# Performance work log

Measured on AMD Instinct MI355X. Metric: run time of the kernel, lower is better.

The kernel has to match this reference:

```python
import jax, jax.numpy as jnp
import numpy as np

P = 524288          # total sampled points
N_RAYS = 4096       # rays
N_FREQ = 5
N_FREQ_VIEW = 3
ACT_SHIFT = float(np.log(1.0 / (1.0 - 0.1) - 1.0))  # alpha_init = 0.1
INTERVAL = 0.5      # stepsize * voxel_size_ratio


def sin_emb(x, n_freq):
    # x: (M,3) -> (M, 3 + 6*n_freq): [x, sin(2^i x), cos(2^i x)]
    freqs = 2.0 ** jnp.arange(n_freq, dtype=x.dtype)
    parts = [x]
    for f in freqs:
        parts.append(jnp.sin(f * x))
        parts.append(jnp.cos(f * x))
    return jnp.concatenate(parts, axis=1)


def _pipeline(sampling_coor, sampling_view, raw_density, ray_id,
              wb0, bb0, wb1, bb1, wb2, bb2,
              wa0, ba0, wa1, ba1, wa2, ba2,
              w_lat, b_lat, w_view, b_view, w_c0, b_c0, w_c1, b_c1):
    relu = jax.nn.relu
    emb = sin_emb(sampling_coor, N_FREQ)                    # (P, 33)
    view_emb = sin_emb(sampling_view, N_FREQ_VIEW)[ray_id]  # (P, 21)
    # Decoder_woslot (K == 1)
    h = relu(emb @ wb0 + bb0)
    h = relu(h @ wb1 + bb1)
    h = relu(h @ wb2 + bb2)
    h = jnp.concatenate([emb, h], axis=1)                   # skip: (P, 97)
    h = relu(h @ wa0 + ba0)
    h = relu(h @ wa1 + ba1)
    h = relu(h @ wa2 + ba2)
    latent = h @ w_lat + b_lat                              # (P, 64)
    hv = relu(jnp.concatenate([latent, view_emb], axis=1) @ w_view + b_view)
    rgb_raw = relu(hv @ w_c0 + b_c0) @ w_c1 + b_c1          # (P, 3)
    rgb = (jnp.tanh(rgb_raw) + 1.0) * 0.5
    sigma = jax.nn.softplus(raw_density[0] + ACT_SHIFT)     # (P,)
    # Raw2Alpha: alpha = 1 - exp(-sigma*interval); hence log(1-alpha) = -sigma*interval
    alpha = 1.0 - jnp.exp(-sigma * INTERVAL)
    log_t = -sigma * INTERVAL
    # Alphas2Weights: per-ray exclusive cumprod of (1-alpha); ray_id is sorted
    cl = jnp.cumsum(log_t)
    excl = cl - log_t                                        # exclusive global cumsum
    base = jax.ops.segment_max(excl, ray_id, num_segments=N_RAYS)  # value at each ray start
    T = jnp.exp(excl - base[ray_id])                         # transmittance
    weights = T * alpha                                      # (P,)
    alphainv_last = jnp.exp(jax.ops.segment_sum(log_t, ray_id, num_segments=N_RAYS))
    # composite with white background
    rgb_marched = (jax.ops.segment_sum(weights[:, None] * rgb, ray_id, num_segments=N_RAYS)
                   + alphainv_last[:, None])
    return rgb_marched                                       # (N_RAYS, 3)


def setup_inputs() -> dict:
    key = jax.random.key(0)
    ks = iter(jax.random.split(key, 40))

    def w(fi, fo):
        return jax.random.normal(next(ks), (fi, fo), jnp.float32) / np.sqrt(fi).astype(np.float32)

    inp = {
        'sampling_coor': jax.random.normal(next(ks), (P, 3), jnp.float32),
        'sampling_view': jax.random.normal(next(ks), (N_RAYS, 3), jnp.float32),
        'raw_density': jax.random.normal(next(ks), (1, P), jnp.float32),
        'ray_id': jnp.sort(jax.random.randint(next(ks), (P,), 0, N_RAYS, jnp.int32)),
        'wb0': w(33, 64), 'bb0': jnp.zeros((64,), jnp.float32),
        'wb1': w(64, 64), 'bb1': jnp.zeros((64,), jnp.float32),
        'wb2': w(64, 64), 'bb2': jnp.zeros((64,), jnp.float32),
        'wa0': w(97, 64), 'ba0': jnp.zeros((64,), jnp.float32),
        'wa1': w(64, 64), 'ba1': jnp.zeros((64,), jnp.float32),
        'wa2': w(64, 64), 'ba2': jnp.zeros((64,), jnp.float32),
        'w_lat': w(64, 64), 'b_lat': jnp.zeros((64,), jnp.float32),
        'w_view': w(85, 32), 'b_view': jnp.zeros((32,), jnp.float32),
        'w_c0': w(32, 16), 'b_c0': jnp.zeros((16,), jnp.float32),
        'w_c1': w(16, 3), 'b_c1': jnp.zeros((3,), jnp.float32),
    }
    return inp


def reference(sampling_coor, sampling_view, raw_density, ray_id,
              wb0, bb0, wb1, bb1, wb2, bb2,
              wa0, ba0, wa1, ba1, wa2, ba2,
              w_lat, b_lat, w_view, b_view, w_c0, b_c0, w_c1, b_c1):
    return _pipeline(sampling_coor, sampling_view, raw_density, ray_id,
                     wb0, bb0, wb1, bb1, wb2, bb2,
                     wa0, ba0, wa1, ba1, wa2, ba2,
                     w_lat, b_lat, w_view, b_view, w_c0, b_c0, w_c1, b_c1)
```

## Files before the change

### kernel.cpp

```cpp
#include <hip/hip_runtime.h>
#include <math.h>

#define NPTS  524288
#define NRAYS 4096
#define ACT_SHIFT_F (-2.1972245773362196f)
#define INTERVAL_F  0.5f

typedef _Float16 f16x8  __attribute__((ext_vector_type(8)));
typedef __fp16   fp16x2 __attribute__((ext_vector_type(2)));
typedef float    f32x4  __attribute__((ext_vector_type(4)));
typedef float    f32x16 __attribute__((ext_vector_type(16)));
typedef int      i32x2  __attribute__((ext_vector_type(2)));
typedef unsigned u32;
typedef unsigned u32x4  __attribute__((ext_vector_type(4)));

#define MFMA32(a,b,c) __builtin_amdgcn_mfma_f32_32x32x16_f16((a),(b),(c),0,0,0)

#define WB0T_OFF   0
#define WB1T_OFF   3072
#define WB2T_OFF   7168
#define WA0T_OFF   11264
#define WA1T_OFF   18432
#define WA2T_OFF   22528
#define WLATT_OFF  26624
#define WVIEWT_OFF 30720
#define WC0T_OFF   33792
#define WEND_H     34816
#define BTAB_H     34816
#define BTAB_F32   384
#define VTAB_OFF   (34816 + 768)
#define RAYTAB_H   (VTAB_OFF + NRAYS*32)
#define PREP_W     34816
#define PREP_BT    (PREP_W + BTAB_F32)
#define PREP_IDS   (PREP_BT + NRAYS)
#define PREP_TOTAL (PREP_IDS + NPTS)

#define SMEM_W (4*128*4 + 128)

__device__ __forceinline__ u32 pk(float a, float b) {
    fp16x2 h = __builtin_amdgcn_cvt_pkrtz(a, b);
    return __builtin_bit_cast(u32, h);
}

__device__ __forceinline__ void plswap(u32 &x, u32 &y) {
    i32x2 r = __builtin_amdgcn_permlane32_swap((int)x, (int)y, false, false);
    x = (u32)r[0]; y = (u32)r[1];
}

__device__ __forceinline__ f32x16 zero16() {
    f32x16 z;
#pragma unroll
    for (int i = 0; i < 16; ++i) z[i] = 0.f;
    return z;
}

template<bool RELU>
__device__ __forceinline__ f16x8 reluq(f16x8 v) {
    if (RELU) {
        f16x8 z = {};
        return __builtin_elementwise_max(v, z);
    }
    return v;
}

template<bool RELU>
__device__ __forceinline__ void d2b(f32x16 a, f16x8 &blo, f16x8 &bhi) {
    u32 p0 = pk(a[0],a[1]),   p1 = pk(a[2],a[3]);
    u32 p2 = pk(a[4],a[5]),   p3 = pk(a[6],a[7]);
    plswap(p0, p2); plswap(p1, p3);
    u32x4 lo = {p0, p1, p2, p3};
    blo = reluq<RELU>(__builtin_bit_cast(f16x8, lo));
    u32 p4 = pk(a[8],a[9]),   p5 = pk(a[10],a[11]);
    u32 p6 = pk(a[12],a[13]), p7 = pk(a[14],a[15]);
    plswap(p4, p6); plswap(p5, p7);
    u32x4 hw = {p4, p5, p6, p7};
    bhi = reluq<RELU>(__builtin_bit_cast(f16x8, hw));
}

extern "C" __global__ void __launch_bounds__(256)
prep_weights(const float* __restrict__ wb0, const float* __restrict__ bb0,
             const float* __restrict__ wb1, const float* __restrict__ bb1,
             const float* __restrict__ wb2, const float* __restrict__ bb2,
             const float* __restrict__ wa0, const float* __restrict__ ba0,
             const float* __restrict__ wa1, const float* __restrict__ ba1,
             const float* __restrict__ wa2, const float* __restrict__ ba2,
             const float* __restrict__ wlat, const float* __restrict__ blat,
             const float* __restrict__ wview, const float* __restrict__ bview,
             const float* __restrict__ wc0, const float* __restrict__ bc0,
             const float* __restrict__ view, const int* __restrict__ ray_id,
             _Float16* __restrict__ pool)
{
    const int id = blockIdx.x * 256 + threadIdx.x;
    if (id >= PREP_TOTAL) return;

    if (id < PREP_W) {
        int r = id; float v = 0.f;
        if (r < 3072) {
            int n = r / 48, k = r % 48;
            if (k < 3) v = wb0[k*64+n]; else if (k == 3) v = bb0[n];
            else if (k < 34) v = wb0[(k-1)*64+n];
        } else if (r < 7168) { r -= 3072; int n=r>>6, k=r&63; v = wb1[k*64+n];
        } else if (r < 11264) { r -= 7168; int n=r>>6, k=r&63; v = wb2[k*64+n];
        } else if (r < 18432) { r -= 11264;
            int n = r / 112, k = r % 112;
            if (k < 3) v = wa0[k*64+n]; else if (k == 3) v = ba0[n];
            else if (k < 34) v = wa0[(k-1)*64+n];
            else if (k >= 48) v = wa0[(k-15)*64+n];
        } else if (r < 22528) { r -= 18432; int n=r>>6, k=r&63; v = wa1[k*64+n];
        } else if (r < 26624) { r -= 22528; int n=r>>6, k=r&63; v = wa2[k*64+n];
        } else if (r < 30720) { r -= 26624; int n=r>>6, k=r&63; v = wlat[k*64+n];
        } else if (r < 33792) { r -= 30720;
            int n = r / 96, k = r % 96;
            if (k < 64) v = wview[k*32+n];
            else { int s = k - 64;
                   if (s < 3) v = wview[(64+s)*32+n];
                   else if (s == 3) v = bview[n];
                   else if (s < 22) v = wview[(63+s)*32+n]; }
        } else { r -= 33792;
            int n = r >> 5, k = r & 31;
            if (n < 16) v = wc0[k*16+n];
        }
        pool[id] = (_Float16)v;
        return;
    }

    if (id < PREP_BT) {
        float* bt = (float*)(pool + BTAB_H);
        const int e = id - PREP_W; float v = 0.f;
        if (e < 320) {
            int l = e >> 6, rem = e & 63;
            int mt = rem >> 5, hi2 = (rem >> 4) & 1, q = rem & 15;
            int row = (q & 3) + 8*(q >> 2) + 4*hi2 + 32*mt;
            const float* src[5] = { bb1, bb2, ba1, ba2, blat };
            v = src[l][row];
        } else if (e < 336) {
            int t = e - 320, hi2 = t >> 3, q = t & 7;
            int row = (q & 3) + 8*(q >> 2) + 4*hi2;
            v = bc0[row];
        }
        bt[e] = v;
        return;
    }

    if (id < PREP_IDS) {
        const int ray = id - PREP_BT;
        const float vx = view[3*ray+0], vy = view[3*ray+1], vz = view[3*ray+2];
        u32 w_[16];
        w_[0] = pk(vx, vy); w_[1] = pk(vz, 1.0f);
#pragma unroll
        for (int f = 0; f < 3; ++f) {
            const float fac = (float)(1 << f);
            float sx = __sinf(fac*vx), cx = __cosf(fac*vx);
            float sy = __sinf(fac*vy), cy = __cosf(fac*vy);
            float sz = __sinf(fac*vz), cz = __cosf(fac*vz);
            w_[2+3*f+0] = pk(sx,sy); w_[2+3*f+1] = pk(sz,cx); w_[2+3*f+2] = pk(cy,cz);
        }
#pragma unroll
        for (int i = 11; i < 16; ++i) w_[i] = 0u;
        u32* dst = (u32*)(pool + VTAB_OFF) + ray * 16;
#pragma unroll
        for (int i = 0; i < 4; ++i)
            ((u32x4*)dst)[i] = (u32x4){w_[4*i], w_[4*i+1], w_[4*i+2], w_[4*i+3]};
        return;
    }

    {
        const int p = id - PREP_IDS;
        int* tab = (int*)(pool + RAYTAB_H);
        const int cur  = ray_id[p];
        const int prev = (p == 0) ? -1 : ray_id[p-1];
        for (int r = prev + 1; r <= cur; ++r) tab[r] = p;
        if (p == NPTS - 1)
            for (int r = cur + 1; r <= NRAYS; ++r) tab[r] = NPTS;
    }
}

template<int NKC, int KPAD>
__device__ __forceinline__ void loadW(f16x8 (&W)[2][4], const _Float16* __restrict__ wT,
                                      int col, int hi) {
#pragma unroll
    for (int mt = 0; mt < 2; ++mt)
#pragma unroll
        for (int kc = 0; kc < NKC; ++kc)
            W[mt][kc] = *(const f16x8*)(wT + (mt*32 + col)*KPAD + kc*16 + hi*8);
}

__device__ __forceinline__ void loadBV(f32x16 (&bv)[2], const float* __restrict__ bt,
                                       int l, int hi) {
#pragma unroll
    for (int mt = 0; mt < 2; ++mt) {
        const float* p = bt + l*64 + (mt*2 + hi)*16;
#pragma unroll
        for (int i = 0; i < 4; ++i) {
            f32x4 v = *(const f32x4*)(p + 4*i);
#pragma unroll
            for (int s = 0; s < 4; ++s) bv[mt][4*i + s] = v[s];
        }
    }
}

template<bool RELU>
__device__ __forceinline__ void dense4(const f16x8 (&W)[2][4], const f32x16 (&bv)[2],
                                       f16x8 (&b)[4][4]) {
#pragma unroll
    for (int t = 0; t < 4; ++t) {
        f32x16 a0 = MFMA32(W[0][0], b[t][0], bv[0]);
        f32x16 a1 = MFMA32(W[1][0], b[t][0], bv[1]);
#pragma unroll
        for (int kc = 1; kc < 4; ++kc) {
            a0 = MFMA32(W[0][kc], b[t][kc], a0);
            a1 = MFMA32(W[1][kc], b[t][kc], a1);
        }
        d2b<RELU>(a0, b[t][0], b[t][1]);
        d2b<RELU>(a1, b[t][2], b[t][3]);
    }
}

extern "C" __global__ void __launch_bounds__(64, 1)
mlp_mfma(const float* __restrict__ coor, const int* __restrict__ ray_id,
         const float* __restrict__ wc1, const float* __restrict__ bc1,
         const _Float16* __restrict__ pool, _Float16* __restrict__ rgb)
{
    __shared__ __align__(16) u32 smem[SMEM_W];
    const int tid   = threadIdx.x;
    const int pbase = blockIdx.x * 128;
    const int col   = tid & 31;
    const int hi    = tid >> 5;

    int rid[4];
#pragma unroll
    for (int t = 0; t < 4; ++t) rid[t] = ray_id[pbase + 32*t + col];

#pragma unroll
    for (int s = 0; s < 2; ++s) {
        const int p  = tid + s*64;
        const int pt = pbase + p;
        const float x = coor[3*pt+0], y = coor[3*pt+1], z = coor[3*pt+2];
        u32 w_[17];
        w_[0] = pk(x, y); w_[1] = pk(z, 1.0f);
#pragma unroll
        for (int f = 0; f < 5; ++f) {
            const float fac = (float)(1 << f);
            float sx = __sinf(fac*x), cx = __cosf(fac*x);
            float sy = __sinf(fac*y), cy = __cosf(fac*y);
            float sz = __sinf(fac*z), cz = __cosf(fac*z);
            w_[2+3*f+0] = pk(sx,sy); w_[2+3*f+1] = pk(sz,cx); w_[2+3*f+2] = pk(cy,cz);
        }
#pragma unroll
        for (int fi = 0; fi < 4; ++fi)
            *(u32x4*)&smem[(fi*128 + p)*4] =
                (u32x4){w_[4*fi], w_[4*fi+1], w_[4*fi+2], w_[4*fi+3]};
        smem[2048 + p] = w_[16];
    }
    __syncthreads();

#define LDE(t, kc) __builtin_bit_cast(f16x8, *(const u32x4*)&smem[(((kc)*2 + hi)*128 + 32*(t) + col)*4])

    const float* bt = (const float*)(pool + BTAB_H);
    const f32x16 Z = zero16();

    f16x8 b[4][4];
    f16x8 WA[2][4], WB[2][4];
    f32x16 bv[2];

    f16x8 E2[4];
#pragma unroll
    for (int t = 0; t < 4; ++t) {
        u32 w16v = smem[2048 + 32*t + col];
        u32x4 e2w = { hi == 0 ? w16v : 0u, 0u, 0u, 0u };
        E2[t] = __builtin_bit_cast(f16x8, e2w);
    }

    loadW<3,48>(WA, pool + WB0T_OFF, col, hi);
    loadW<4,64>(WB, pool + WB1T_OFF, col, hi);

#pragma unroll
    for (int t = 0; t < 4; ++t) {
        f16x8 e0 = LDE(t, 0), e1 = LDE(t, 1);
        f32x16 a0 = MFMA32(WA[0][0], e0, Z);
        f32x16 a1 = MFMA32(WA[1][0], e0, Z);
        a0 = MFMA32(WA[0][1], e1, a0);
        a1 = MFMA32(WA[1][1], e1, a1);
        a0 = MFMA32(WA[0][2], E2[t], a0);
        a1 = MFMA32(WA[1][2], E2[t], a1);
        d2b<true>(a0, b[t][0], b[t][1]);
        d2b<true>(a1, b[t][2], b[t][3]);
    }

    loadW<4,64>(WA, pool + WB2T_OFF, col, hi);
    loadBV(bv, bt, 0, hi);
    dense4<true>(WB, bv, b);

    loadW<3,112>(WB, pool + WA0T_OFF, col, hi);
    loadBV(bv, bt, 1, hi);
    dense4<true>(WA, bv, b);

    loadW<4,112>(WA, pool + WA0T_OFF + 48, col, hi);
#pragma unroll
    for (int t = 0; t < 4; ++t) {
        f16x8 e0 = LDE(t, 0), e1 = LDE(t, 1);
        f32x16 a0 = MFMA32(WB[0][0], e0, Z);
        f32x16 a1 = MFMA32(WB[1][0], e0, Z);
        a0 = MFMA32(WB[0][1], e1, a0);
        a1 = MFMA32(WB[1][1], e1, a1);
        a0 = MFMA32(WB[0][2], E2[t], a0);
        a1 = MFMA32(WB[1][2], E2[t], a1);
#pragma unroll
        for (int kc = 0; kc < 4; ++kc) {
            a0 = MFMA32(WA[0][kc], b[t][kc], a0);
            a1 = MFMA32(WA[1][kc], b[t][kc], a1);
        }
        d2b<true>(a0, b[t][0], b[t][1]);
        d2b<true>(a1, b[t][2], b[t][3]);
    }

    loadW<4,64>(WB, pool + WA1T_OFF, col, hi);
    loadBV(bv, bt, 2, hi);
    dense4<true>(WB, bv, b);

    loadW<4,64>(WA, pool + WA2T_OFF, col, hi);
    loadBV(bv, bt, 3, hi);
    dense4<true>(WA, bv, b);

    const _Float16* vtab = pool + VTAB_OFF;
    f16x8 VE[4][2];
#pragma unroll
    for (int t = 0; t < 4; ++t)
#pragma unroll
        for (int kc = 0; kc < 2; ++kc)
            VE[t][kc] = *(const f16x8*)(vtab + rid[t]*32 + kc*16 + hi*8);

    loadW<4,64>(WB, pool + WLATT_OFF, col, hi);
    loadBV(bv, bt, 4, hi);
    dense4<false>(WB, bv, b);

    {
        f16x8 Wv[6];
#pragma unroll
        for (int kc = 0; kc < 6; ++kc)
            Wv[kc] = *(const f16x8*)(pool + WVIEWT_OFF + col*96 + kc*16 + hi*8);
#pragma unroll
        for (int t = 0; t < 4; ++t) {
            f32x16 a = MFMA32(Wv[0], b[t][0], Z);
#pragma unroll
            for (int kc = 1; kc < 4; ++kc) a = MFMA32(Wv[kc], b[t][kc], a);
            a = MFMA32(Wv[4], VE[t][0], a);
            a = MFMA32(Wv[5], VE[t][1], a);
            d2b<true>(a, b[t][0], b[t][1]);
        }
    }

    {
        f16x8 Wc[2];
#pragma unroll
        for (int kc = 0; kc < 2; ++kc)
            Wc[kc] = *(const f16x8*)(pool + WC0T_OFF + col*32 + kc*16 + hi*8);

        f32x16 C = zero16();
        {
            f32x4 c0a = *(const f32x4*)(bt + 320 + hi*8);
            f32x4 c0b = *(const f32x4*)(bt + 320 + hi*8 + 4);
#pragma unroll
            for (int s = 0; s < 4; ++s) { C[s] = c0a[s]; C[4+s] = c0b[s]; }
        }

        float wl[24];
        {
            f32x4 w0 = *(const f32x4*)(wc1 + 12*hi);
            f32x4 w1 = *(const f32x4*)(wc1 + 12*hi + 4);
            f32x4 w2 = *(const f32x4*)(wc1 + 12*hi + 8);
            f32x4 w3 = *(const f32x4*)(wc1 + 24 + 12*hi);
            f32x4 w4 = *(const f32x4*)(wc1 + 24 + 12*hi + 4);
            f32x4 w5 = *(const f32x4*)(wc1 + 24 + 12*hi + 8);
#pragma unroll
            for (int s = 0; s < 4; ++s) {
                wl[s]    = w0[s]; wl[4+s]  = w1[s]; wl[8+s]  = w2[s];
                wl[12+s] = w3[s]; wl[16+s] = w4[s]; wl[20+s] = w5[s];
            }
        }
        const float bo0 = bc1[0], bo1 = bc1[1], bo2 = bc1[2];

#pragma unroll
        for (int t = 0; t < 4; ++t) {
            f32x16 a = MFMA32(Wc[0], b[t][0], C);
            a = MFMA32(Wc[1], b[t][1], a);
            float hc[8];
#pragma unroll
            for (int i = 0; i < 8; ++i) hc[i] = fmaxf(a[i], 0.f);

            float r0 = 0.f, r1 = 0.f, r2 = 0.f;
#pragma unroll
            for (int q = 0; q < 4; ++q) {
                r0 = fmaf(hc[q], wl[3*q+0], fmaf(hc[4+q], wl[12+3*q+0], r0));
                r1 = fmaf(hc[q], wl[3*q+1], fmaf(hc[4+q], wl[12+3*q+1], r1));
                r2 = fmaf(hc[q], wl[3*q+2], fmaf(hc[4+q], wl[12+3*q+2], r2));
            }
            r0 += __shfl_xor(r0, 32);
            r1 += __shfl_xor(r1, 32);
            r2 += __shfl_xor(r2, 32);
            if (hi == 0) {
                const float K2 = 2.8853900817779268f;
                float e0 = exp2f(K2 * (r0 + bo0));
                float e1 = exp2f(K2 * (r1 + bo1));
                float e2 = exp2f(K2 * (r2 + bo2));
                float v0 = 1.f - __builtin_amdgcn_rcpf(e0 + 1.f);
                float v1 = 1.f - __builtin_amdgcn_rcpf(e1 + 1.f);
                float v2 = 1.f - __builtin_amdgcn_rcpf(e2 + 1.f);
                const int pt = pbase + 32*t + col;
                rgb[3*pt+0] = (_Float16)v0;
                rgb[3*pt+1] = (_Float16)v1;
                rgb[3*pt+2] = (_Float16)v2;
            }
        }
    }
#undef LDE
}

extern "C" __global__ void __launch_bounds__(256)
composite(const float* __restrict__ raw_density,
          const int*   __restrict__ rtab,
          const _Float16* __restrict__ rgb,
          float*       __restrict__ out)
{
    const int lane = threadIdx.x & 63;
    const int ray  = blockIdx.x * 4 + (threadIdx.x >> 6);

    const int start = rtab[ray];
    const int end   = rtab[ray + 1];

    float carry = 0.0f, a0 = 0.0f, a1 = 0.0f, a2 = 0.0f;

    for (int base = start; base < end; base += 64) {
        const int  idx   = base + lane;
        const bool valid = idx < end;

        float lt = 0.0f, alpha = 0.0f;
        if (valid) {
            const float xx  = raw_density[idx] + ACT_SHIFT_F;
            const float sig = fmaxf(xx, 0.0f) + log1pf(expf(-fabsf(xx)));
            lt    = -sig * INTERVAL_F;
            alpha = 1.0f - expf(lt);
        }

        float incl = lt;
#pragma unroll
        for (int d = 1; d < 64; d <<= 1) {
            const float n = __shfl_up(incl, d);
            if (lane >= d) incl += n;
        }

        const float T = expf(carry + (incl - lt));
        if (valid) {
            const float w = T * alpha;
            a0 = fmaf(w, (float)rgb[3*idx+0], a0);
            a1 = fmaf(w, (float)rgb[3*idx+1], a1);
            a2 = fmaf(w, (float)rgb[3*idx+2], a2);
        }
        carry += __shfl(incl, 63);
    }

#pragma unroll
    for (int d = 32; d > 0; d >>= 1) {
        a0 += __shfl_xor(a0, d);
        a1 += __shfl_xor(a1, d);
        a2 += __shfl_xor(a2, d);
    }

    if (lane == 0) {
        const float ainv = expf(carry);
        out[3*ray+0] = a0 + ainv;
        out[3*ray+1] = a1 + ainv;
        out[3*ray+2] = a2 + ainv;
    }
}

extern "C" void kernel_launch(void* const* d_in, const int* in_sizes, int n_in,
                              void* d_out, int out_size, void* d_ws, size_t ws_size,
                              hipStream_t stream) {
    const float* coor        = (const float*)d_in[0];
    const float* view        = (const float*)d_in[1];
    const float* raw_density = (const float*)d_in[2];
    const int*   ray_id      = (const int*)  d_in[3];
    const float* wb0  = (const float*)d_in[4];  const float* bb0  = (const float*)d_in[5];
    const float* wb1  = (const float*)d_in[6];  const float* bb1  = (const float*)d_in[7];
    const float* wb2  = (const float*)d_in[8];  const float* bb2  = (const float*)d_in[9];
    const float* wa0  = (const float*)d_in[10]; const float* ba0  = (const float*)d_in[11];
    const float* wa1  = (const float*)d_in[12]; const float* ba1  = (const float*)d_in[13];
    const float* wa2  = (const float*)d_in[14]; const float* ba2  = (const float*)d_in[15];
    const float* wlat = (const float*)d_in[16]; const float* blat = (const float*)d_in[17];
    const float* wvw  = (const float*)d_in[18]; const float* bvw  = (const float*)d_in[19];
    const float* wc0  = (const float*)d_in[20]; const float* bc0  = (const float*)d_in[21];
    const float* wc1  = (const float*)d_in[22]; const float* bc1  = (const float*)d_in[23];

    _Float16* rgb  = (_Float16*)d_ws;
    _Float16* pool = (_Float16*)((char*)d_ws + (size_t)NPTS * 3 * 2);
    const int* rtab = (const int*)(pool + RAYTAB_H);

    prep_weights<<<(PREP_TOTAL + 255) / 256, 256, 0, stream>>>(
        wb0, bb0, wb1, bb1, wb2, bb2, wa0, ba0, wa1, ba1, wa2, ba2,
        wlat, blat, wvw, bvw, wc0, bc0, view, ray_id, pool);

    mlp_mfma<<<NPTS / 128, 64, 0, stream>>>(
        coor, ray_id, wc1, bc1, pool, rgb);

    composite<<<NRAYS / 4, 256, 0, stream>>>(raw_density, rtab, rgb, (float*)d_out);
}
```

Baseline: 63.77 us.

## Stage padded MLP weights in LDS shared by four waves per block

The MLP kernel now uses 256-thread blocks (four waves, 128 points each). Each block copies the padded fp16 weights of the first seven layers into LDS once, and every wave reads its MFMA operands from there instead of reloading them from global memory. Weight rows are padded (stride 34 or 58 u32) to avoid LDS bank conflicts. Embedding operands are now built in registers with permlane swaps instead of going through shared memory. The cost is about 64KB of LDS per block and an initial copy plus barrier, which may limit occupancy.

```diff
diff --git a/kernel.cpp b/kernel.cpp
--- a/kernel.cpp
+++ b/kernel.cpp
@@ -12,30 +12,41 @@
 typedef float    f32x16 __attribute__((ext_vector_type(16)));
 typedef int      i32x2  __attribute__((ext_vector_type(2)));
 typedef unsigned u32;
+typedef unsigned u32x2  __attribute__((ext_vector_type(2)));
 typedef unsigned u32x4  __attribute__((ext_vector_type(4)));
 
 #define MFMA32(a,b,c) __builtin_amdgcn_mfma_f32_32x32x16_f16((a),(b),(c),0,0,0)
 
-#define WB0T_OFF   0
-#define WB1T_OFF   3072
-#define WB2T_OFF   7168
-#define WA0T_OFF   11264
-#define WA1T_OFF   18432
-#define WA2T_OFF   22528
-#define WLATT_OFF  26624
-#define WVIEWT_OFF 30720
-#define WC0T_OFF   33792
-#define WEND_H     34816
-#define BTAB_H     34816
-#define BTAB_F32   384
-#define VTAB_OFF   (34816 + 768)
-#define RAYTAB_H   (VTAB_OFF + NRAYS*32)
-#define PREP_W     34816
-#define PREP_BT    (PREP_W + BTAB_F32)
-#define PREP_IDS   (PREP_BT + NRAYS)
+#define WB0_H    0
+#define WB1_H    3328
+#define WB2_H    7680
+#define WA0_H    12032
+#define WA1_H    19456
+#define WA2_H    23808
+#define WLAT_H   28160
+#define WLDS_H   32512
+#define WVIEW_H  32512
+#define WC0_H    35584
+#define WEND_H   36608
+#define BTAB_H   36608
+#define VTAB_H   37376
+#define RAYTAB_H 168448
+#define PREP_W    36608
+#define PREP_BT   (PREP_W + 384)
+#define PREP_IDS  (PREP_BT + NRAYS)
 #define PREP_TOTAL (PREP_IDS + NPTS)
 
-#define SMEM_W (4*128*4 + 128)
+#define S2_WB0 26
+#define S2_D   34
+#define S2_WA0 58
+#define U_WB0  0
+#define U_WB1  1664
+#define U_WB2  3840
+#define U_WA0  6016
+#define U_WA1  9728
+#define U_WA2  11904
+#define U_WLAT 14080
+#define LDS_U32 16256
 
 __device__ __forceinline__ u32 pk(float a, float b) {
     fp16x2 h = __builtin_amdgcn_cvt_pkrtz(a, b);
@@ -75,6 +86,13 @@
     plswap(p4, p6); plswap(p5, p7);
     u32x4 hw = {p4, p5, p6, p7};
     bhi = reluq<RELU>(__builtin_bit_cast(f16x8, hw));
+}
+
+__device__ __forceinline__ f16x8 ldw(const u32* __restrict__ sw, int u) {
+    u32x2 a = *(const u32x2*)(sw + u);
+    u32x2 b = *(const u32x2*)(sw + u + 2);
+    u32x4 r = {a[0], a[1], b[0], b[1]};
+    return __builtin_bit_cast(f16x8, r);
 }
 
 extern "C" __global__ void __launch_bounds__(256)
@@ -95,28 +113,33 @@
 
     if (id < PREP_W) {
         int r = id; float v = 0.f;
-        if (r < 3072) {
-            int n = r / 48, k = r % 48;
+        if (r < 3328) {
+            int n = r / 52, k = r % 52;
             if (k < 3) v = wb0[k*64+n]; else if (k == 3) v = bb0[n];
             else if (k < 34) v = wb0[(k-1)*64+n];
-        } else if (r < 7168) { r -= 3072; int n=r>>6, k=r&63; v = wb1[k*64+n];
-        } else if (r < 11264) { r -= 7168; int n=r>>6, k=r&63; v = wb2[k*64+n];
-        } else if (r < 18432) { r -= 11264;
-            int n = r / 112, k = r % 112;
+        } else if (r < 7680) { r -= 3328;
+            int n = r / 68, k = r % 68; if (k < 64) v = wb1[k*64+n];
+        } else if (r < 12032) { r -= 7680;
+            int n = r / 68, k = r % 68; if (k < 64) v = wb2[k*64+n];
+        } else if (r < 19456) { r -= 12032;
+            int n = r / 116, k = r % 116;
             if (k < 3) v = wa0[k*64+n]; else if (k == 3) v = ba0[n];
             else if (k < 34) v = wa0[(k-1)*64+n];
-            else if (k >= 48) v = wa0[(k-15)*64+n];
-        } else if (r < 22528) { r -= 18432; int n=r>>6, k=r&63; v = wa1[k*64+n];
-        } else if (r < 26624) { r -= 22528; int n=r>>6, k=r&63; v = wa2[k*64+n];
-        } else if (r < 30720) { r -= 26624; int n=r>>6, k=r&63; v = wlat[k*64+n];
-        } else if (r < 33792) { r -= 30720;
+            else if (k >= 48 && k < 112) v = wa0[(k-15)*64+n];
+        } else if (r < 23808) { r -= 19456;
+            int n = r / 68, k = r % 68; if (k < 64) v = wa1[k*64+n];
+        } else if (r < 28160) { r -= 23808;
+            int n = r / 68, k = r % 68; if (k < 64) v = wa2[k*64+n];
+        } else if (r < 32512) { r -= 28160;
+            int n = r / 68, k = r % 68; if (k < 64) v = wlat[k*64+n];
+        } else if (r < 35584) { r -= 32512;
             int n = r / 96, k = r % 96;
             if (k < 64) v = wview[k*32+n];
             else { int s = k - 64;
                    if (s < 3) v = wview[(64+s)*32+n];
                    else if (s == 3) v = bview[n];
                    else if (s < 22) v = wview[(63+s)*32+n]; }
-        } else { r -= 33792;
+        } else { r -= 35584;
             int n = r >> 5, k = r & 31;
             if (n < 16) v = wc0[k*16+n];
         }
@@ -157,7 +180,7 @@
         }
 #pragma unroll
         for (int i = 11; i < 16; ++i) w_[i] = 0u;
-        u32* dst = (u32*)(pool + VTAB_OFF) + ray * 16;
+        u32* dst = (u32*)(pool + VTAB_H) + ray * 16;
 #pragma unroll
         for (int i = 0; i < 4; ++i)
             ((u32x4*)dst)[i] = (u32x4){w_[4*i], w_[4*i+1], w_[4*i+2], w_[4*i+3]};
@@ -175,16 +198,6 @@
     }
 }
 
-template<int NKC, int KPAD>
-__device__ __forceinline__ void loadW(f16x8 (&W)[2][4], const _Float16* __restrict__ wT,
-                                      int col, int hi) {
-#pragma unroll
-    for (int mt = 0; mt < 2; ++mt)
-#pragma unroll
-        for (int kc = 0; kc < NKC; ++kc)
-            W[mt][kc] = *(const f16x8*)(wT + (mt*32 + col)*KPAD + kc*16 + hi*8);
-}
-
 __device__ __forceinline__ void loadBV(f32x16 (&bv)[2], const float* __restrict__ bt,
                                        int l, int hi) {
 #pragma unroll
@@ -200,8 +213,15 @@
 }
 
 template<bool RELU>
-__device__ __forceinline__ void dense4(const f16x8 (&W)[2][4], const f32x16 (&bv)[2],
-                                       f16x8 (&b)[4][4]) {
+__device__ __forceinline__ void denseL(const u32* __restrict__ sw, int base,
+                                       const f32x16 (&bv)[2], f16x8 (&b)[4][4],
+                                       int col, int hi) {
+    f16x8 W[2][4];
+#pragma unroll
+    for (int mt = 0; mt < 2; ++mt)
+#pragma unroll
+        for (int kc = 0; kc < 4; ++kc)
+            W[mt][kc] = ldw(sw, base + (mt*32 + col)*S2_D + kc*8 + hi*4);
 #pragma unroll
     for (int t = 0; t < 4; ++t) {
         f32x16 a0 = MFMA32(W[0][0], b[t][0], bv[0]);
@@ -216,25 +236,34 @@
     }
 }
 
-extern "C" __global__ void __launch_bounds__(64, 1)
+extern "C" __global__ void __launch_bounds__(256, 2)
 mlp_mfma(const float* __restrict__ coor, const int* __restrict__ ray_id,
          const float* __restrict__ wc1, const float* __restrict__ bc1,
          const _Float16* __restrict__ pool, _Float16* __restrict__ rgb)
 {
-    __shared__ __align__(16) u32 smem[SMEM_W];
-    const int tid   = threadIdx.x;
-    const int pbase = blockIdx.x * 128;
-    const int col   = tid & 31;
-    const int hi    = tid >> 5;
+    __shared__ __align__(16) u32 sw[LDS_U32];
+    const int tid  = threadIdx.x;
+    const int lane = tid & 63;
+    const int wv   = tid >> 6;
+    const int col  = lane & 31;
+    const int hi   = lane >> 5;
+    const int wbase = blockIdx.x * 512 + wv * 128;
+
+    {
+        const u32x4* pw = (const u32x4*)pool;
+        u32x4* dw = (u32x4*)sw;
+#pragma unroll 4
+        for (int i = tid; i < LDS_U32/4; i += 256) dw[i] = pw[i];
+    }
 
     int rid[4];
 #pragma unroll
-    for (int t = 0; t < 4; ++t) rid[t] = ray_id[pbase + 32*t + col];
-
+    for (int t = 0; t < 4; ++t) rid[t] = ray_id[wbase + 32*t + col];
+
+    f16x8 E[4][3];
 #pragma unroll
     for (int s = 0; s < 2; ++s) {
-        const int p  = tid + s*64;
-        const int pt = pbase + p;
+        const int pt = wbase + s*64 + lane;
         const float x = coor[3*pt+0], y = coor[3*pt+1], z = coor[3*pt+2];
         u32 w_[17];
         w_[0] = pk(x, y); w_[1] = pk(z, 1.0f);
@@ -247,82 +276,92 @@
             w_[2+3*f+0] = pk(sx,sy); w_[2+3*f+1] = pk(sz,cx); w_[2+3*f+2] = pk(cy,cz);
         }
 #pragma unroll
-        for (int fi = 0; fi < 4; ++fi)
-            *(u32x4*)&smem[(fi*128 + p)*4] =
-                (u32x4){w_[4*fi], w_[4*fi+1], w_[4*fi+2], w_[4*fi+3]};
-        smem[2048 + p] = w_[16];
+        for (int kc = 0; kc < 2; ++kc) {
+            u32 xw[4], yw[4];
+#pragma unroll
+            for (int i = 0; i < 4; ++i) {
+                xw[i] = w_[kc*8 + i]; yw[i] = w_[kc*8 + 4 + i];
+                plswap(xw[i], yw[i]);
+            }
+            u32x4 lo = {xw[0], xw[1], xw[2], xw[3]};
+            u32x4 hw = {yw[0], yw[1], yw[2], yw[3]};
+            E[2*s  ][kc] = __builtin_bit_cast(f16x8, lo);
+            E[2*s+1][kc] = __builtin_bit_cast(f16x8, hw);
+        }
+        u32 X = w_[16], Y = 0u;
+        plswap(X, Y);
+        u32x4 e2a = {X, 0u, 0u, 0u}, e2b = {Y, 0u, 0u, 0u};
+        E[2*s  ][2] = __builtin_bit_cast(f16x8, e2a);
+        E[2*s+1][2] = __builtin_bit_cast(f16x8, e2b);
     }
     __syncthreads();
-
-#define LDE(t, kc) __builtin_bit_cast(f16x8, *(const u32x4*)&smem[(((kc)*2 + hi)*128 + 32*(t) + col)*4])
 
     const float* bt = (const float*)(pool + BTAB_H);
     const f32x16 Z = zero16();
 
     f16x8 b[4][4];
-    f16x8 WA[2][4], WB[2][4];
     f32x16 bv[2];
 
-    f16x8 E2[4];
-#pragma unroll
-    for (int t = 0; t < 4; ++t) {
-        u32 w16v = smem[2048 + 32*t + col];
-        u32x4 e2w = { hi == 0 ? w16v : 0u, 0u, 0u, 0u };
-        E2[t] = __builtin_bit_cast(f16x8, e2w);
-    }
-
-    loadW<3,48>(WA, pool + WB0T_OFF, col, hi);
-    loadW<4,64>(WB, pool + WB1T_OFF, col, hi);
-
-#pragma unroll
-    for (int t = 0; t < 4; ++t) {
-        f16x8 e0 = LDE(t, 0), e1 = LDE(t, 1);
-        f32x16 a0 = MFMA32(WA[0][0], e0, Z);
-        f32x16 a1 = MFMA32(WA[1][0], e0, Z);
-        a0 = MFMA32(WA[0][1], e1, a0);
-        a1 = MFMA32(WA[1][1], e1, a1);
-        a0 = MFMA32(WA[0][2], E2[t], a0);
-        a1 = MFMA32(WA[1][2], E2[t], a1);
-        d2b<true>(a0, b[t][0], b[t][1]);
-        d2b<true>(a1, b[t][2], b[t][3]);
-    }
-
-    loadW<4,64>(WA, pool + WB2T_OFF, col, hi);
+    {
+        f16x8 W[2][3];
+#pragma unroll
+        for (int mt = 0; mt < 2; ++mt)
+#pragma unroll
+            for (int kc = 0; kc < 3; ++kc)
+                W[mt][kc] = ldw(sw, U_WB0 + (mt*32 + col)*S2_WB0 + kc*8 + hi*4);
+#pragma unroll
+        for (int t = 0; t < 4; ++t) {
+            f32x16 a0 = MFMA32(W[0][0], E[t][0], Z);
+            f32x16 a1 = MFMA32(W[1][0], E[t][0], Z);
+            a0 = MFMA32(W[0][1], E[t][1], a0);
+            a1 = MFMA32(W[1][1], E[t][1], a1);
+            a0 = MFMA32(W[0][2], E[t][2], a0);
+            a1 = MFMA32(W[1][2], E[t][2], a1);
+            d2b<true>(a0, b[t][0], b[t][1]);
+            d2b<true>(a1, b[t][2], b[t][3]);
+        }
+    }
+
     loadBV(bv, bt, 0, hi);
-    dense4<true>(WB, bv, b);
-
-    loadW<3,112>(WB, pool + WA0T_OFF, col, hi);
+    denseL<true>(sw, U_WB1, bv, b, col, hi);
     loadBV(bv, bt, 1, hi);
-    dense4<true>(WA, bv, b);
-
-    loadW<4,112>(WA, pool + WA0T_OFF + 48, col, hi);
-#pragma unroll
-    for (int t = 0; t < 4; ++t) {
-        f16x8 e0 = LDE(t, 0), e1 = LDE(t, 1);
-        f32x16 a0 = MFMA32(WB[0][0], e0, Z);
-        f32x16 a1 = MFMA32(WB[1][0], e0, Z);
-        a0 = MFMA32(WB[0][1], e1, a0);
-        a1 = MFMA32(WB[1][1], e1, a1);
-        a0 = MFMA32(WB[0][2], E2[t], a0);
-        a1 = MFMA32(WB[1][2], E2[t], a1);
-#pragma unroll
-        for (int kc = 0; kc < 4; ++kc) {
-            a0 = MFMA32(WA[0][kc], b[t][kc], a0);
-            a1 = MFMA32(WA[1][kc], b[t][kc], a1);
-        }
-        d2b<true>(a0, b[t][0], b[t][1]);
-        d2b<true>(a1, b[t][2], b[t][3]);
-    }
-
-    loadW<4,64>(WB, pool + WA1T_OFF, col, hi);
+    denseL<true>(sw, U_WB2, bv, b, col, hi);
+
+    {
+        f16x8 We[2][3], Wh[2][4];
+#pragma unroll
+        for (int mt = 0; mt < 2; ++mt) {
+#pragma unroll
+            for (int kc = 0; kc < 3; ++kc)
+                We[mt][kc] = ldw(sw, U_WA0 + (mt*32 + col)*S2_WA0 + kc*8 + hi*4);
+#pragma unroll
+            for (int kc = 0; kc < 4; ++kc)
+                Wh[mt][kc] = ldw(sw, U_WA0 + (mt*32 + col)*S2_WA0 + 24 + kc*8 + hi*4);
+        }
+#pragma unroll
+        for (int t = 0; t < 4; ++t) {
+            f32x16 a0 = MFMA32(We[0][0], E[t][0], Z);
+            f32x16 a1 = MFMA32(We[1][0], E[t][0], Z);
+            a0 = MFMA32(We[0][1], E[t][1], a0);
+            a1 = MFMA32(We[1][1], E[t][1], a1);
+            a0 = MFMA32(We[0][2], E[t][2], a0);
+            a1 = MFMA32(We[1][2], E[t][2], a1);
+#pragma unroll
+            for (int kc = 0; kc < 4; ++kc) {
+                a0 = MFMA32(Wh[0][kc], b[t][kc], a0);
+                a1 = MFMA32(Wh[1][kc], b[t][kc], a1);
+            }
+            d2b<true>(a0, b[t][0], b[t][1]);
+            d2b<true>(a1, b[t][2], b[t][3]);
+        }
+    }
+
     loadBV(bv, bt, 2, hi);
-    dense4<true>(WB, bv, b);
-
-    loadW<4,64>(WA, pool + WA2T_OFF, col, hi);
+    denseL<true>(sw, U_WA1, bv, b, col, hi);
     loadBV(bv, bt, 3, hi);
-    dense4<true>(WA, bv, b);
-
-    const _Float16* vtab = pool + VTAB_OFF;
+    denseL<true>(sw, U_WA2, bv, b, col, hi);
+
+    const _Float16* vtab = pool + VTAB_H;
     f16x8 VE[4][2];
 #pragma unroll
     for (int t = 0; t < 4; ++t)
@@ -330,15 +369,14 @@
         for (int kc = 0; kc < 2; ++kc)
             VE[t][kc] = *(const f16x8*)(vtab + rid[t]*32 + kc*16 + hi*8);
 
-    loadW<4,64>(WB, pool + WLATT_OFF, col, hi);
     loadBV(bv, bt, 4, hi);
-    dense4<false>(WB, bv, b);
+    denseL<false>(sw, U_WLAT, bv, b, col, hi);
 
     {
         f16x8 Wv[6];
 #pragma unroll
         for (int kc = 0; kc < 6; ++kc)
-            Wv[kc] = *(const f16x8*)(pool + WVIEWT_OFF + col*96 + kc*16 + hi*8);
+            Wv[kc] = *(const f16x8*)(pool + WVIEW_H + col*96 + kc*16 + hi*8);
 #pragma unroll
         for (int t = 0; t < 4; ++t) {
             f32x16 a = MFMA32(Wv[0], b[t][0], Z);
@@ -354,7 +392,7 @@
         f16x8 Wc[2];
 #pragma unroll
         for (int kc = 0; kc < 2; ++kc)
-            Wc[kc] = *(const f16x8*)(pool + WC0T_OFF + col*32 + kc*16 + hi*8);
+            Wc[kc] = *(const f16x8*)(pool + WC0_H + col*32 + kc*16 + hi*8);
 
         f32x16 C = zero16();
         {
@@ -406,14 +444,13 @@
                 float v0 = 1.f - __builtin_amdgcn_rcpf(e0 + 1.f);
                 float v1 = 1.f - __builtin_amdgcn_rcpf(e1 + 1.f);
                 float v2 = 1.f - __builtin_amdgcn_rcpf(e2 + 1.f);
-                const int pt = pbase + 32*t + col;
+                const int pt = wbase + 32*t + col;
                 rgb[3*pt+0] = (_Float16)v0;
                 rgb[3*pt+1] = (_Float16)v1;
                 rgb[3*pt+2] = (_Float16)v2;
             }
         }
     }
-#undef LDE
 }
 
 extern "C" __global__ void __launch_bounds__(256)
@@ -500,7 +537,7 @@
         wb0, bb0, wb1, bb1, wb2, bb2, wa0, ba0, wa1, ba1, wa2, ba2,
         wlat, blat, wvw, bvw, wc0, bc0, view, ray_id, pool);
 
-    mlp_mfma<<<NPTS / 128, 64, 0, stream>>>(
+    mlp_mfma<<<NPTS / 512, 256, 0, stream>>>(
         coor, ray_id, wc1, bc1, pool, rgb);
 
     composite<<<NRAYS / 4, 256, 0, stream>>>(raw_density, rtab, rgb, (float*)d_out);
```

Result: faster. 52.71 us (-17.3%).
